# Performance work log

Measured on AMD Instinct MI355X. Metric: run time of the kernel, lower is better.

## Reference

```python
import jax, jax.numpy as jnp
import numpy as np

N = 100000      # nodes
E = 1600000     # edges (before self-loops)
IN_C = 128
HID = 256
L = 4
EPS = 1e-5


def setup_inputs() -> dict:
    key = jax.random.key(0)
    ks = jax.random.split(key, 12)
    s = 0.05
    x = jax.random.normal(ks[0], (N, IN_C), dtype=jnp.float32)
    edge_index = jax.random.randint(ks[1], (2, E), 0, N, dtype=jnp.int64)
    enc_w = jax.random.normal(ks[2], (IN_C, HID), dtype=jnp.float32) * s
    enc_b = jnp.zeros((HID,), jnp.float32)
    conv_w = jax.random.normal(ks[3], (L, HID, HID), dtype=jnp.float32) * s
    conv_b = jnp.zeros((L, HID), jnp.float32)
    ln_g = jnp.ones((L, HID), jnp.float32)
    ln_b = jnp.zeros((L, HID), jnp.float32)
    lin1_w = jax.random.normal(ks[4], (HID, HID // 2), dtype=jnp.float32) * s
    lin1_b = jnp.zeros((HID // 2,), jnp.float32)
    lin2_w = jax.random.normal(ks[5], (HID // 2, 1), dtype=jnp.float32) * s
    lin2_b = jnp.zeros((1,), jnp.float32)
    return dict(x=x, edge_index=edge_index, enc_w=enc_w, enc_b=enc_b,
                conv_w=conv_w, conv_b=conv_b, ln_g=ln_g, ln_b=ln_b,
                lin1_w=lin1_w, lin1_b=lin1_b, lin2_w=lin2_w, lin2_b=lin2_b)


def _layer_norm(h, g, b):
    mu = jnp.mean(h, axis=-1, keepdims=True)
    var = jnp.mean(jnp.square(h - mu), axis=-1, keepdims=True)
    return (h - mu) * jax.lax.rsqrt(var + EPS) * g + b


def reference(x, edge_index, enc_w, enc_b, conv_w, conv_b, ln_g, ln_b,
              lin1_w, lin1_b, lin2_w, lin2_b):
    loops = jnp.arange(N, dtype=edge_index.dtype)
    row = jnp.concatenate([edge_index[0], loops])   # source
    col = jnp.concatenate([edge_index[1], loops])   # target
    # GCN symmetric norm with self-loop weight 1 (improved=False)
    deg = jax.ops.segment_sum(jnp.ones(row.shape[0], jnp.float32), col,
                              num_segments=N)
    dis = jnp.where(deg > 0, jax.lax.rsqrt(deg), 0.0)  # deg^-1/2, [N]

    h = x @ enc_w + enc_b
    for i in range(L):
        hw = h @ conv_w[i]
        # norm_e = dis[row]*dis[col]: scale at source, aggregate, scale at target
        agg = jax.ops.segment_sum((hw * dis[:, None])[row], col,
                                  num_segments=N)
        h = agg * dis[:, None] + conv_b[i]
        h = jax.nn.relu(_layer_norm(h, ln_g[i], ln_b[i]))
        # dropout p=0.1 is identity in eval mode
    h = jax.nn.relu(h @ lin1_w + lin1_b)
    return h @ lin2_w + lin2_b  # [N, 1]
```

## Files before the change

### kernel.cpp

```cpp
#include <hip/hip_runtime.h>

#define N_NODES 100000
#define N_EDGES 1600000
#define IN_C    128
#define HID     256
#define NLAYER  4

#define NBUCK 391
#define BCAP  8192
#define EPB   4096
#define CAPL  6144

typedef __attribute__((ext_vector_type(8))) __bf16 bf16x8;
typedef __attribute__((ext_vector_type(4))) float  floatx4;
typedef __attribute__((ext_vector_type(2))) float  floatx2;

__device__ inline unsigned short f2b(float f) {
    unsigned u = __builtin_bit_cast(unsigned, f);
    return (unsigned short)((u + 0x7fffu + ((u >> 16) & 1u)) >> 16);
}
__device__ inline floatx2 pkadd(floatx2 x, floatx2 y) {
    floatx2 r;
    asm("v_pk_add_f32 %0, %1, %2" : "=v"(r) : "v"(x), "v"(y));
    return r;
}
__device__ inline void acc8p(floatx2* a, uint4 v) {
    unsigned wds[4] = {v.x, v.y, v.z, v.w};
    #pragma unroll
    for (int k = 0; k < 4; ++k) {
        floatx2 x;
        x[0] = __builtin_bit_cast(float, wds[k] << 16);
        x[1] = __builtin_bit_cast(float, wds[k] & 0xffff0000u);
        a[k] = pkadd(a[k], x);
    }
}
__device__ inline void gl16(const void* g, void* l) {
    __builtin_amdgcn_global_load_lds(
        (const __attribute__((address_space(1))) unsigned int*)g,
        (__attribute__((address_space(3))) unsigned int*)l, 16, 0, 0);
}

__global__ __launch_bounds__(256) void kb_scatter(
        const int* __restrict__ row, const int* __restrict__ col,
        int* __restrict__ gfill, unsigned* __restrict__ pairs, int e) {
    __shared__ unsigned sp[EPB];
    __shared__ unsigned short sbk[EPB];
    __shared__ int hist[NBUCK];
    __shared__ int lpre[NBUCK];
    __shared__ int lbase[NBUCK];
    __shared__ int wsum[4];
    __shared__ int carry;
    const int tid = threadIdx.x, lane = tid & 63, w = tid >> 6;
    const int base = blockIdx.x * EPB;
    const int nv   = min(EPB, e - base);
    for (int b = tid; b < NBUCK; b += 256) hist[b] = 0;
    __syncthreads();
    #pragma unroll
    for (int k = 0; k < EPB / 256; ++k) {
        int i = base + k * 256 + tid;
        if (i < e) atomicAdd(&hist[((unsigned)col[i]) >> 8], 1);
    }
    __syncthreads();
    for (int b = tid; b < NBUCK; b += 256) {
        int h = hist[b];
        lbase[b] = h ? atomicAdd(&gfill[b], h) : 0;
    }
    {
        int v = hist[tid];
        int inc = v;
        #pragma unroll
        for (int o = 1; o < 64; o <<= 1) { int u = __shfl_up(inc, o); if (lane >= o) inc += u; }
        if (lane == 63) wsum[w] = inc;
        __syncthreads();
        if (tid == 0) { int r = 0; for (int i = 0; i < 4; ++i) { int x = wsum[i]; wsum[i] = r; r += x; } carry = r; }
        __syncthreads();
        lpre[tid] = wsum[w] + inc - v;
        int c0 = carry;
        __syncthreads();
        int idx = 256 + tid;
        int v1 = (idx < NBUCK) ? hist[idx] : 0;
        int inc1 = v1;
        #pragma unroll
        for (int o = 1; o < 64; o <<= 1) { int u = __shfl_up(inc1, o); if (lane >= o) inc1 += u; }
        if (lane == 63) wsum[w] = inc1;
        __syncthreads();
        if (tid == 0) { int r = 0; for (int i = 0; i < 4; ++i) { int x = wsum[i]; wsum[i] = r; r += x; } }
        __syncthreads();
        if (idx < NBUCK) lpre[idx] = c0 + wsum[w] + inc1 - v1;
    }
    __syncthreads();
    for (int b = tid; b < NBUCK; b += 256) hist[b] = 0;
    __syncthreads();
    #pragma unroll
    for (int k = 0; k < EPB / 256; ++k) {
        int i = base + k * 256 + tid;
        if (i < e) {
            unsigned cv = (unsigned)col[i];
            int bk = cv >> 8;
            int q = lpre[bk] + atomicAdd(&hist[bk], 1);
            sp[q]  = ((unsigned)row[i] << 8) | (cv & 255u);
            sbk[q] = (unsigned short)bk;
        }
    }
    __syncthreads();
    for (int i = tid; i < nv; i += 256) {
        int bk = sbk[i];
        int pos = lbase[bk] + (i - lpre[bk]);
        if (pos < BCAP) pairs[(size_t)bk * BCAP + pos] = sp[i];
    }
}

__global__ __launch_bounds__(256) void kb_build(
        const unsigned* __restrict__ pairs, const int* __restrict__ gfill,
        int* __restrict__ offs, float* __restrict__ dis,
        int* __restrict__ srcl, int n) {
    __shared__ int lcnt[256];
    __shared__ int lstart[256];
    __shared__ int wsum[4];
    __shared__ int sbase;
    __shared__ int sl[CAPL];
    const int b = blockIdx.x;
    const int tid = threadIdx.x, lane = tid & 63, w = tid >> 6;
    int cnt = gfill[b]; if (cnt > CAPL) cnt = CAPL;
    const unsigned* bp = pairs + (size_t)b * BCAP;
    int pa = 0;
    for (int i = tid; i < b; i += 256) pa += gfill[i];
    #pragma unroll
    for (int o = 1; o < 64; o <<= 1) pa += __shfl_xor(pa, o);
    lcnt[tid] = 0;
    if (lane == 0) wsum[w] = pa;
    __syncthreads();
    if (tid == 0) sbase = wsum[0] + wsum[1] + wsum[2] + wsum[3];
    for (int i = tid; i < cnt; i += 256)
        atomicAdd(&lcnt[bp[i] & 255u], 1);
    __syncthreads();
    const int base = sbase;
    int v = lcnt[tid];
    int inc = v;
    #pragma unroll
    for (int o = 1; o < 64; o <<= 1) { int u = __shfl_up(inc, o); if (lane >= o) inc += u; }
    if (lane == 63) wsum[w] = inc;
    __syncthreads();
    if (tid == 0) { int r = 0; for (int i = 0; i < 4; ++i) { int x = wsum[i]; wsum[i] = r; r += x; } }
    __syncthreads();
    int excl = wsum[w] + inc - v;
    lstart[tid] = excl;
    int node = (b << 8) + tid;
    if (node < n) {
        dis[node]  = rsqrtf((float)(v + 1));
        offs[node] = base + excl;
    }
    __syncthreads();
    lcnt[tid] = 0;
    __syncthreads();
    for (int i = tid; i < cnt; i += 256) {
        unsigned pr = bp[i];
        int c = pr & 255u;
        int q = lstart[c] + atomicAdd(&lcnt[c], 1);
        sl[q] = (int)(pr >> 8);
    }
    __syncthreads();
    for (int i = tid; i < cnt; i += 256)
        srcl[base + i] = sl[i];
}

__global__ void k_wtz(const float* __restrict__ enc_w, const float* __restrict__ conv_w,
                      const float* __restrict__ w1,
                      unsigned short* __restrict__ enc_t, unsigned short* __restrict__ conv_t,
                      unsigned short* __restrict__ lin1_t, int* __restrict__ gfill,
                      int* __restrict__ offs) {
    int idx = blockIdx.x * blockDim.x + threadIdx.x;
    if (idx == 0) offs[N_NODES] = N_EDGES;
    if (idx < NBUCK) gfill[idx] = 0;
    if (idx < IN_C * HID) {
        int k = idx / HID, n = idx % HID;
        enc_t[n * IN_C + k] = f2b(enc_w[idx]);
    } else if (idx < IN_C * HID + NLAYER * HID * HID) {
        int r = idx - IN_C * HID;
        int l = r / (HID * HID);
        int e = r % (HID * HID);
        int k = e / HID, n = e % HID;
        conv_t[(size_t)l * HID * HID + n * HID + k] = f2b(conv_w[r]);
    } else if (idx < IN_C * HID + NLAYER * HID * HID + HID * (HID / 2)) {
        int e = idx - (IN_C * HID + NLAYER * HID * HID);
        int k = e / (HID / 2), n = e % (HID / 2);
        lin1_t[n * HID + k] = f2b(w1[e]);
    }
}

__global__ __launch_bounds__(512) void k_mme(
        const float* __restrict__ Af,
        const unsigned short* __restrict__ Wt,
        const float* __restrict__ bias,
        unsigned short* __restrict__ Cout, int M) {
    const int K = IN_C;
    __shared__ unsigned short As[128 * 32];
    __shared__ unsigned short Bs[256 * 32];
    const int tid  = threadIdx.x;
    const int lane = tid & 63;
    const int w    = tid >> 6;
    const int bm   = blockIdx.x * 128;

    const int r0 = tid >> 2, q0 = tid & 3;
    const int a_off  = min(bm + r0, M - 1) * K + q0 * 8;
    const int b_off0 = r0 * K + q0 * 8;
    const int b_off1 = (r0 + 128) * K + q0 * 8;

    floatx4 acc[4][4];
    #pragma unroll
    for (int i = 0; i < 4; ++i)
        #pragma unroll
        for (int j = 0; j < 4; ++j)
            acc[i][j] = (floatx4){0.f, 0.f, 0.f, 0.f};

    const int wm = (w & 1) * 64;
    const int wn = (w >> 1) * 64;
    const int fm = lane & 15;
    const int fq = (lane >> 4) * 8;

    uint4 ra;
    auto loadA = [&](int koff, uint4& oa) {
        float4 f0 = *(const float4*)(Af + a_off + koff);
        float4 f1 = *(const float4*)(Af + a_off + koff + 4);
        oa.x = (unsigned)f2b(f0.x) | ((unsigned)f2b(f0.y) << 16);
        oa.y = (unsigned)f2b(f0.z) | ((unsigned)f2b(f0.w) << 16);
        oa.z = (unsigned)f2b(f1.x) | ((unsigned)f2b(f1.y) << 16);
        oa.w = (unsigned)f2b(f1.z) | ((unsigned)f2b(f1.w) << 16);
    };

    loadA(0, ra);

    const int KT = K >> 5;
    for (int kt = 0; kt < KT; ++kt) {
        int k0 = kt << 5;
        ((uint4*)As)[tid] = ra;
        gl16(Wt + b_off0 + k0, Bs + (size_t)tid * 8);
        gl16(Wt + b_off1 + k0, Bs + (size_t)(tid + 512) * 8);
        __syncthreads();
        if (kt + 1 < KT) loadA((kt + 1) << 5, ra);
        bf16x8 af[4], bfr[4];
        #pragma unroll
        for (int i = 0; i < 4; ++i)
            af[i] = *(const bf16x8*)(const void*)(As + (wm + i * 16 + fm) * 32 + fq);
        #pragma unroll
        for (int j = 0; j < 4; ++j)
            bfr[j] = *(const bf16x8*)(const void*)(Bs + (wn + j * 16 + fm) * 32 + fq);
        #pragma unroll
        for (int i = 0; i < 4; ++i)
            #pragma unroll
            for (int j = 0; j < 4; ++j)
                acc[i][j] = __builtin_amdgcn_mfma_f32_16x16x32_bf16(af[i], bfr[j], acc[i][j], 0, 0, 0);
        __syncthreads();
    }

    const int quad = lane >> 4;
    #pragma unroll
    for (int i = 0; i < 4; ++i) {
        #pragma unroll
        for (int r = 0; r < 4; ++r) {
            int row = bm + wm + i * 16 + quad * 4 + r;
            if (row >= M) continue;
            #pragma unroll
            for (int j = 0; j < 4; ++j) {
                int colg = wn + j * 16 + fm;
                float v = acc[i][j][r] + bias[colg];
                Cout[(size_t)row * HID + colg] = f2b(v);
            }
        }
    }
}

__global__ __launch_bounds__(512) void k_mmc(
        const unsigned short* __restrict__ A,
        const unsigned short* __restrict__ Wt,
        const float* __restrict__ scale,
        unsigned short* __restrict__ Cout, int M) {
    const int K = HID;
    __shared__ unsigned short As[128 * 32];
    __shared__ unsigned short Bs[256 * 32];
    const int tid  = threadIdx.x;
    const int lane = tid & 63;
    const int w    = tid >> 6;
    const int bm   = blockIdx.x * 128;

    const int r0 = tid >> 2, q0 = tid & 3;
    const int a_off  = min(bm + r0, M - 1) * K + q0 * 8;
    const int b_off0 = r0 * K + q0 * 8;
    const int b_off1 = (r0 + 128) * K + q0 * 8;

    floatx4 acc[4][4];
    #pragma unroll
    for (int i = 0; i < 4; ++i)
        #pragma unroll
        for (int j = 0; j < 4; ++j)
            acc[i][j] = (floatx4){0.f, 0.f, 0.f, 0.f};

    const int wm = (w & 1) * 64;
    const int wn = (w >> 1) * 64;
    const int fm = lane & 15;
    const int fq = (lane >> 4) * 8;

    for (int kt = 0; kt < 8; ++kt) {
        int k0 = kt << 5;
        gl16(A  + a_off  + k0, As + (size_t)tid * 8);
        gl16(Wt + b_off0 + k0, Bs + (size_t)tid * 8);
        gl16(Wt + b_off1 + k0, Bs + (size_t)(tid + 512) * 8);
        __syncthreads();
        bf16x8 af[4], bfr[4];
        #pragma unroll
        for (int i = 0; i < 4; ++i)
            af[i] = *(const bf16x8*)(const void*)(As + (wm + i * 16 + fm) * 32 + fq);
        #pragma unroll
        for (int j = 0; j < 4; ++j)
            bfr[j] = *(const bf16x8*)(const void*)(Bs + (wn + j * 16 + fm) * 32 + fq);
        #pragma unroll
        for (int i = 0; i < 4; ++i)
            #pragma unroll
            for (int j = 0; j < 4; ++j)
                acc[i][j] = __builtin_amdgcn_mfma_f32_16x16x32_bf16(af[i], bfr[j], acc[i][j], 0, 0, 0);
        __syncthreads();
    }

    const int quad = lane >> 4;
    #pragma unroll
    for (int i = 0; i < 4; ++i) {
        #pragma unroll
        for (int r = 0; r < 4; ++r) {
            int row = bm + wm + i * 16 + quad * 4 + r;
            if (row >= M) continue;
            float sc = scale[row];
            #pragma unroll
            for (int j = 0; j < 4; ++j) {
                int colg = wn + j * 16 + fm;
                Cout[(size_t)row * HID + colg] = f2b(acc[i][j][r] * sc);
            }
        }
    }
}

__global__ __launch_bounds__(256) void k_head(
        const unsigned short* __restrict__ A,
        const unsigned short* __restrict__ Wt,
        const float* __restrict__ b1, const float* __restrict__ w2,
        const float* __restrict__ b2, float* __restrict__ out, int M) {
    const int K = 256;
    __shared__ unsigned short As[128 * 32];
    __shared__ unsigned short Bs[128 * 32];
    const int tid  = threadIdx.x;
    const int lane = tid & 63;
    const int w    = tid >> 6;
    const int bm   = blockIdx.x * 128;

    const int i0 = tid, i1 = tid + 256;
    const int r0 = i0 >> 2, r1 = i1 >> 2;
    const int q0 = i0 & 3,  q1 = i1 & 3;
    const int a_off0 = min(bm + r0, M - 1) * K + q0 * 8;
    const int a_off1 = min(bm + r1, M - 1) * K + q1 * 8;
    const int b_off0 = r0 * K + q0 * 8;
    const int b_off1 = r1 * K + q1 * 8;

    floatx4 acc[4][4];
    #pragma unroll
    for (int i = 0; i < 4; ++i)
        #pragma unroll
        for (int j = 0; j < 4; ++j)
            acc[i][j] = (floatx4){0.f, 0.f, 0.f, 0.f};

    const int wm = (w & 1) * 64;
    const int wn = (w >> 1) * 64;
    const int fm = lane & 15;
    const int fq = (lane >> 4) * 8;

    for (int kt = 0; kt < 8; ++kt) {
        int k0 = kt << 5;
        gl16(A  + a_off0 + k0, As + (size_t)i0 * 8);
        gl16(A  + a_off1 + k0, As + (size_t)i1 * 8);
        gl16(Wt + b_off0 + k0, Bs + (size_t)i0 * 8);
        gl16(Wt + b_off1 + k0, Bs + (size_t)i1 * 8);
        __syncthreads();
        bf16x8 af[4], bfr[4];
        #pragma unroll
        for (int i = 0; i < 4; ++i)
            af[i] = *(const bf16x8*)(const void*)(As + (wm + i * 16 + fm) * 32 + fq);
        #pragma unroll
        for (int j = 0; j < 4; ++j)
            bfr[j] = *(const bf16x8*)(const void*)(Bs + (wn + j * 16 + fm) * 32 + fq);
        #pragma unroll
        for (int i = 0; i < 4; ++i)
            #pragma unroll
            for (int j = 0; j < 4; ++j)
                acc[i][j] = __builtin_amdgcn_mfma_f32_16x16x32_bf16(af[i], bfr[j], acc[i][j], 0, 0, 0);
        __syncthreads();
    }

    float* red = (float*)As;
    const int q = lane >> 4;
    float b1v[4], w2v[4];
    #pragma unroll
    for (int j = 0; j < 4; ++j) {
        int col = wn + j * 16 + fm;
        b1v[j] = b1[col]; w2v[j] = w2[col];
    }
    #pragma unroll
    for (int i = 0; i < 4; ++i) {
        #pragma unroll
        for (int r = 0; r < 4; ++r) {
            float s = 0.f;
            #pragma unroll
            for (int j = 0; j < 4; ++j)
                s += fmaxf(acc[i][j][r] + b1v[j], 0.f) * w2v[j];
            #pragma unroll
            for (int off = 1; off < 16; off <<= 1) s += __shfl_xor(s, off);
            if (fm == 0) {
                int m = wm + i * 16 + q * 4 + r;
                red[m * 2 + (wn >> 6)] = s;
            }
        }
    }
    __syncthreads();
    if (tid < 128) {
        int row = bm + tid;
        if (row < M) out[row] = red[tid * 2] + red[tid * 2 + 1] + b2[0];
    }
}

__global__ void k_agg(const unsigned short* __restrict__ hw, const int* __restrict__ srcl,
                      const int* __restrict__ offs, const float* __restrict__ dis,
                      const float* __restrict__ cb, const float* __restrict__ g,
                      const float* __restrict__ bt, unsigned short* __restrict__ hout, int n) {
    int gtid = blockIdx.x * blockDim.x + threadIdx.x;
    int node = __builtin_amdgcn_readfirstlane(gtid >> 6);
    int lane = threadIdx.x & 63;
    const int half = lane >> 5;
    const int sub  = lane & 31;
    const uint4* T = (const uint4*)hw;

    floatx2 a2[4], c2[4];
    #pragma unroll
    for (int k = 0; k < 4; ++k) { a2[k] = (floatx2)0.f; c2[k] = (floatx2)0.f; }
    if (half == 0)
        acc8p(a2, T[(size_t)node * 32 + sub]);

    int p = offs[node], pe = offs[node + 1];
    if (p + 7 < pe) {
        uint4 va, vb, vc, vd;
        {
            int s0 = srcl[p],     s1 = srcl[p + 1], s2 = srcl[p + 2], s3 = srcl[p + 3];
            int s4 = srcl[p + 4], s5 = srcl[p + 5], s6 = srcl[p + 6], s7 = srcl[p + 7];
            int ea = half ? s1 : s0, eb = half ? s3 : s2;
            int ec = half ? s5 : s4, ed = half ? s7 : s6;
            va = T[(size_t)ea * 32 + sub]; vb = T[(size_t)eb * 32 + sub];
            vc = T[(size_t)ec * 32 + sub]; vd = T[(size_t)ed * 32 + sub];
        }
        for (p += 8; p + 7 < pe; p += 8) {
            int s0 = srcl[p],     s1 = srcl[p + 1], s2 = srcl[p + 2], s3 = srcl[p + 3];
            int s4 = srcl[p + 4], s5 = srcl[p + 5], s6 = srcl[p + 6], s7 = srcl[p + 7];
            int ea = half ? s1 : s0, eb = half ? s3 : s2;
            int ec = half ? s5 : s4, ed = half ? s7 : s6;
            uint4 wa = T[(size_t)ea * 32 + sub];
            uint4 wb = T[(size_t)eb * 32 + sub];
            uint4 wc = T[(size_t)ec * 32 + sub];
            uint4 wd = T[(size_t)ed * 32 + sub];
            acc8p(a2, va); acc8p(c2, vb); acc8p(a2, vc); acc8p(c2, vd);
            va = wa; vb = wb; vc = wc; vd = wd;
        }
        acc8p(a2, va); acc8p(c2, vb); acc8p(a2, vc); acc8p(c2, vd);
    }
    for (; p + 1 < pe; p += 2) {
        int s0 = srcl[p], s1 = srcl[p + 1];
        int ea = half ? s1 : s0;
        acc8p(a2, T[(size_t)ea * 32 + sub]);
    }
    if (p < pe && half == 0)
        acc8p(a2, T[(size_t)srcl[p] * 32 + sub]);

    float af[8];
    #pragma unroll
    for (int k = 0; k < 4; ++k) {
        floatx2 t = pkadd(a2[k], c2[k]);
        af[2 * k]     = t[0] + __shfl_xor(t[0], 32);
        af[2 * k + 1] = t[1] + __shfl_xor(t[1], 32);
    }
    float dc = dis[node];
    const float4* cb4 = (const float4*)cb;
    const float4* g4  = (const float4*)g;
    const float4* bt4 = (const float4*)bt;
    float4 cba = cb4[sub * 2], cbb = cb4[sub * 2 + 1];
    float h[8];
    h[0] = fmaf(af[0], dc, cba.x); h[1] = fmaf(af[1], dc, cba.y);
    h[2] = fmaf(af[2], dc, cba.z); h[3] = fmaf(af[3], dc, cba.w);
    h[4] = fmaf(af[4], dc, cbb.x); h[5] = fmaf(af[5], dc, cbb.y);
    h[6] = fmaf(af[6], dc, cbb.z); h[7] = fmaf(af[7], dc, cbb.w);
    float s = 0.f, sq = 0.f;
    #pragma unroll
    for (int j = 0; j < 8; ++j) { s += h[j]; sq += h[j] * h[j]; }
    #pragma unroll
    for (int off = 1; off < 32; off <<= 1) { s += __shfl_xor(s, off); sq += __shfl_xor(sq, off); }
    float mu  = s * (1.f / 256.f);
    float var = sq * (1.f / 256.f) - mu * mu;
    float inv = rsqrtf(var + 1e-5f);
    if (half == 0) {
        float4 ga = g4[sub * 2], gb = g4[sub * 2 + 1];
        float4 ba = bt4[sub * 2], bb = bt4[sub * 2 + 1];
        float gv[8] = {ga.x, ga.y, ga.z, ga.w, gb.x, gb.y, gb.z, gb.w};
        float bv[8] = {ba.x, ba.y, ba.z, ba.w, bb.x, bb.y, bb.z, bb.w};
        unsigned short o[8];
        #pragma unroll
        for (int j = 0; j < 8; ++j)
            o[j] = f2b(fmaxf(fmaf((h[j] - mu) * inv, gv[j], bv[j]), 0.f));
        uint4 st;
        st.x = (unsigned)o[0] | ((unsigned)o[1] << 16);
        st.y = (unsigned)o[2] | ((unsigned)o[3] << 16);
        st.z = (unsigned)o[4] | ((unsigned)o[5] << 16);
        st.w = (unsigned)o[6] | ((unsigned)o[7] << 16);
        ((uint4*)hout)[(size_t)node * 32 + sub] = st;
    }
}

extern "C" void kernel_launch(void* const* d_in, const int* in_sizes, int n_in,
                              void* d_out, int out_size, void* d_ws, size_t ws_size,
                              hipStream_t stream) {
    const float* x      = (const float*)d_in[0];
    const int*   ei     = (const int*)d_in[1];
    const float* enc_w  = (const float*)d_in[2];
    const float* enc_b  = (const float*)d_in[3];
    const float* conv_w = (const float*)d_in[4];
    const float* conv_b = (const float*)d_in[5];
    const float* ln_g   = (const float*)d_in[6];
    const float* ln_b   = (const float*)d_in[7];
    const float* w1     = (const float*)d_in[8];
    const float* b1     = (const float*)d_in[9];
    const float* w2     = (const float*)d_in[10];
    const float* b2     = (const float*)d_in[11];
    float* out = (float*)d_out;

    char* ws = (char*)d_ws;
    size_t off = 0;
    auto alloc = [&](size_t bytes) -> void* {
        void* p = ws + off;
        off = (off + bytes + 255) & ~(size_t)255;
        return p;
    };
    int*   offs  = (int*)alloc((size_t)(N_NODES + 1) * 4);
    int*   srcl  = (int*)alloc((size_t)N_EDGES * 4);
    float* dis   = (float*)alloc((size_t)N_NODES * 4);
    int*   gfill = (int*)alloc((size_t)NBUCK * 4);
    unsigned short* hb = (unsigned short*)alloc((size_t)N_NODES * HID * 2);
    unsigned short* hw = (unsigned short*)alloc((size_t)N_NODES * HID * 2);
    unsigned* pairs = (unsigned*)alloc((size_t)NBUCK * BCAP * 4);
    unsigned short* enc_t  = (unsigned short*)alloc((size_t)IN_C * HID * 2);
    unsigned short* conv_t = (unsigned short*)alloc((size_t)NLAYER * HID * HID * 2);
    unsigned short* lin1_t = (unsigned short*)alloc((size_t)HID * (HID / 2) * 2);

    const int* row = ei;
    const int* col = ei + N_EDGES;

    {
        int tot = IN_C * HID + NLAYER * HID * HID + HID * (HID / 2);
        k_wtz<<<(tot + 255) / 256, 256, 0, stream>>>(enc_w, conv_w, w1,
                                                     enc_t, conv_t, lin1_t, gfill, offs);
    }
    kb_scatter<<<(N_EDGES + EPB - 1) / EPB, 256, 0, stream>>>(row, col, gfill, pairs, N_EDGES);
    kb_build<<<NBUCK, 256, 0, stream>>>(pairs, gfill, offs, dis, srcl, N_NODES);

    k_mme<<<(N_NODES + 127) / 128, 512, 0, stream>>>(x, enc_t, enc_b, hb, N_NODES);

    for (int l = 0; l < NLAYER; ++l) {
        k_mmc<<<(N_NODES + 127) / 128, 512, 0, stream>>>(
            hb, conv_t + (size_t)l * HID * HID, dis, hw, N_NODES);
        k_agg<<<(N_NODES * 64 + 255) / 256, 256, 0, stream>>>(
            hw, srcl, offs, dis, conv_b + l * HID, ln_g + l * HID, ln_b + l * HID, hb, N_NODES);
    }

    k_head<<<(N_NODES + 127) / 128, 256, 0, stream>>>(hb, lin1_t, b1, w2, b2, out, N_NODES);
}
```

Baseline: 787.2 us.

## Fuse aggregation+LayerNorm with next layer's GEMM via LDS-resident tile

Adds a k_fused kernel that gathers neighbor rows, applies bias, LayerNorm and ReLU for a 128-node tile, and stores the bf16 result in a swizzled 64 KB LDS tile. It then multiplies that tile by the next layer's weights with MFMA and writes the dis-scaled output. This removes the global write and re-read of the intermediate h between the aggregation and GEMM kernels for layers 1-3, using ping-pong buffers. The cost is lower occupancy from the large LDS footprint, and the gather phase runs one wave per node, serialized over 16 rows per block, which may hide gather latency less well than the standalone aggregation kernel.

```diff
diff --git a/kernel.cpp b/kernel.cpp
--- a/kernel.cpp
+++ b/kernel.cpp
@@ -338,6 +338,167 @@
     }
 }
 
+__global__ __launch_bounds__(512, 4) void k_fused(
+        const unsigned short* __restrict__ hwin, const int* __restrict__ srcl,
+        const int* __restrict__ offs, const float* __restrict__ dis,
+        const float* __restrict__ cb, const float* __restrict__ g,
+        const float* __restrict__ bt,
+        const unsigned short* __restrict__ Wt,
+        unsigned short* __restrict__ hwout, int M) {
+    __shared__ unsigned short As2[128 * 256];
+    __shared__ unsigned short Bs[256 * 32];
+    const int tid  = threadIdx.x;
+    const int lane = tid & 63;
+    const int w    = tid >> 6;
+    const int bm   = blockIdx.x * 128;
+    const int half = lane >> 5;
+    const int sub  = lane & 31;
+    const uint4* T = (const uint4*)hwin;
+    const float4* cb4 = (const float4*)cb;
+    const float4* g4  = (const float4*)g;
+    const float4* bt4 = (const float4*)bt;
+
+    for (int rr = 0; rr < 16; ++rr) {
+        const int nloc = rr * 8 + w;
+        const int node = bm + nloc;
+        if (node < M) {
+            floatx2 a2[4], c2[4];
+            #pragma unroll
+            for (int k = 0; k < 4; ++k) { a2[k] = (floatx2)0.f; c2[k] = (floatx2)0.f; }
+            if (half == 0)
+                acc8p(a2, T[(size_t)node * 32 + sub]);
+            int p = offs[node], pe = offs[node + 1];
+            if (p + 7 < pe) {
+                uint4 va, vb, vc, vd;
+                {
+                    int s0 = srcl[p],     s1 = srcl[p + 1], s2 = srcl[p + 2], s3 = srcl[p + 3];
+                    int s4 = srcl[p + 4], s5 = srcl[p + 5], s6 = srcl[p + 6], s7 = srcl[p + 7];
+                    int ea = half ? s1 : s0, eb = half ? s3 : s2;
+                    int ec = half ? s5 : s4, ed = half ? s7 : s6;
+                    va = T[(size_t)ea * 32 + sub]; vb = T[(size_t)eb * 32 + sub];
+                    vc = T[(size_t)ec * 32 + sub]; vd = T[(size_t)ed * 32 + sub];
+                }
+                for (p += 8; p + 7 < pe; p += 8) {
+                    int s0 = srcl[p],     s1 = srcl[p + 1], s2 = srcl[p + 2], s3 = srcl[p + 3];
+                    int s4 = srcl[p + 4], s5 = srcl[p + 5], s6 = srcl[p + 6], s7 = srcl[p + 7];
+                    int ea = half ? s1 : s0, eb = half ? s3 : s2;
+                    int ec = half ? s5 : s4, ed = half ? s7 : s6;
+                    uint4 wa = T[(size_t)ea * 32 + sub];
+                    uint4 wb = T[(size_t)eb * 32 + sub];
+                    uint4 wc = T[(size_t)ec * 32 + sub];
+                    uint4 wd = T[(size_t)ed * 32 + sub];
+                    acc8p(a2, va); acc8p(c2, vb); acc8p(a2, vc); acc8p(c2, vd);
+                    va = wa; vb = wb; vc = wc; vd = wd;
+                }
+                acc8p(a2, va); acc8p(c2, vb); acc8p(a2, vc); acc8p(c2, vd);
+            }
+            for (; p + 1 < pe; p += 2) {
+                int s0 = srcl[p], s1 = srcl[p + 1];
+                int ea = half ? s1 : s0;
+                acc8p(a2, T[(size_t)ea * 32 + sub]);
+            }
+            if (p < pe && half == 0)
+                acc8p(a2, T[(size_t)srcl[p] * 32 + sub]);
+
+            float af8[8];
+            #pragma unroll
+            for (int k = 0; k < 4; ++k) {
+                floatx2 t = pkadd(a2[k], c2[k]);
+                af8[2 * k]     = t[0] + __shfl_xor(t[0], 32);
+                af8[2 * k + 1] = t[1] + __shfl_xor(t[1], 32);
+            }
+            float dc = dis[node];
+            float4 cba = cb4[sub * 2], cbb = cb4[sub * 2 + 1];
+            float h[8];
+            h[0] = fmaf(af8[0], dc, cba.x); h[1] = fmaf(af8[1], dc, cba.y);
+            h[2] = fmaf(af8[2], dc, cba.z); h[3] = fmaf(af8[3], dc, cba.w);
+            h[4] = fmaf(af8[4], dc, cbb.x); h[5] = fmaf(af8[5], dc, cbb.y);
+            h[6] = fmaf(af8[6], dc, cbb.z); h[7] = fmaf(af8[7], dc, cbb.w);
+            float s = 0.f, sq = 0.f;
+            #pragma unroll
+            for (int j = 0; j < 8; ++j) { s += h[j]; sq += h[j] * h[j]; }
+            #pragma unroll
+            for (int off = 1; off < 32; off <<= 1) { s += __shfl_xor(s, off); sq += __shfl_xor(sq, off); }
+            float mu  = s * (1.f / 256.f);
+            float var = sq * (1.f / 256.f) - mu * mu;
+            float inv = rsqrtf(var + 1e-5f);
+            if (half == 0) {
+                float4 ga = g4[sub * 2], gb = g4[sub * 2 + 1];
+                float4 ba = bt4[sub * 2], bb = bt4[sub * 2 + 1];
+                float gv[8] = {ga.x, ga.y, ga.z, ga.w, gb.x, gb.y, gb.z, gb.w};
+                float bv[8] = {ba.x, ba.y, ba.z, ba.w, bb.x, bb.y, bb.z, bb.w};
+                unsigned short o[8];
+                #pragma unroll
+                for (int j = 0; j < 8; ++j)
+                    o[j] = f2b(fmaxf(fmaf((h[j] - mu) * inv, gv[j], bv[j]), 0.f));
+                uint4 st;
+                st.x = (unsigned)o[0] | ((unsigned)o[1] << 16);
+                st.y = (unsigned)o[2] | ((unsigned)o[3] << 16);
+                st.z = (unsigned)o[4] | ((unsigned)o[5] << 16);
+                st.w = (unsigned)o[6] | ((unsigned)o[7] << 16);
+                unsigned byte = ((unsigned)(nloc * 512 + sub * 16)) ^ (((unsigned)nloc & 7u) << 4);
+                *(uint4*)((char*)As2 + byte) = st;
+            }
+        }
+    }
+    __syncthreads();
+
+    const int r0 = tid >> 2, q0 = tid & 3;
+    const int b_off0 = r0 * 256 + q0 * 8;
+    const int b_off1 = (r0 + 128) * 256 + q0 * 8;
+
+    floatx4 acc[4][4];
+    #pragma unroll
+    for (int i = 0; i < 4; ++i)
+        #pragma unroll
+        for (int j = 0; j < 4; ++j)
+            acc[i][j] = (floatx4){0.f, 0.f, 0.f, 0.f};
+
+    const int wm = (w & 1) * 64;
+    const int wn = (w >> 1) * 64;
+    const int fm = lane & 15;
+    const int fq = (lane >> 4) * 8;
+
+    for (int kt = 0; kt < 8; ++kt) {
+        int k0 = kt << 5;
+        gl16(Wt + b_off0 + k0, Bs + (size_t)tid * 8);
+        gl16(Wt + b_off1 + k0, Bs + (size_t)(tid + 512) * 8);
+        __syncthreads();
+        bf16x8 af[4], bfr[4];
+        #pragma unroll
+        for (int i = 0; i < 4; ++i) {
+            int row = wm + i * 16 + fm;
+            unsigned byte = ((unsigned)(row * 512 + kt * 64 + fq * 2)) ^ (((unsigned)row & 7u) << 4);
+            af[i] = *(const bf16x8*)(const void*)((const char*)As2 + byte);
+        }
+        #pragma unroll
+        for (int j = 0; j < 4; ++j)
+            bfr[j] = *(const bf16x8*)(const void*)(Bs + (wn + j * 16 + fm) * 32 + fq);
+        #pragma unroll
+        for (int i = 0; i < 4; ++i)
+            #pragma unroll
+            for (int j = 0; j < 4; ++j)
+                acc[i][j] = __builtin_amdgcn_mfma_f32_16x16x32_bf16(af[i], bfr[j], acc[i][j], 0, 0, 0);
+        __syncthreads();
+    }
+
+    const int quad = lane >> 4;
+    #pragma unroll
+    for (int i = 0; i < 4; ++i) {
+        #pragma unroll
+        for (int r = 0; r < 4; ++r) {
+            int row = bm + wm + i * 16 + quad * 4 + r;
+            if (row >= M) continue;
+            float sc = dis[row];
+            #pragma unroll
+            for (int j = 0; j < 4; ++j) {
+                int colg = wn + j * 16 + fm;
+                hwout[(size_t)row * HID + colg] = f2b(acc[i][j][r] * sc);
+            }
+        }
+    }
+}
+
 __global__ __launch_bounds__(256) void k_head(
         const unsigned short* __restrict__ A,
         const unsigned short* __restrict__ Wt,
@@ -474,12 +635,12 @@
     if (p < pe && half == 0)
         acc8p(a2, T[(size_t)srcl[p] * 32 + sub]);
 
-    float af[8];
+    float af8[8];
     #pragma unroll
     for (int k = 0; k < 4; ++k) {
         floatx2 t = pkadd(a2[k], c2[k]);
-        af[2 * k]     = t[0] + __shfl_xor(t[0], 32);
-        af[2 * k + 1] = t[1] + __shfl_xor(t[1], 32);
+        af8[2 * k]     = t[0] + __shfl_xor(t[0], 32);
+        af8[2 * k + 1] = t[1] + __shfl_xor(t[1], 32);
     }
     float dc = dis[node];
     const float4* cb4 = (const float4*)cb;
@@ -487,10 +648,10 @@
     const float4* bt4 = (const float4*)bt;
     float4 cba = cb4[sub * 2], cbb = cb4[sub * 2 + 1];
     float h[8];
-    h[0] = fmaf(af[0], dc, cba.x); h[1] = fmaf(af[1], dc, cba.y);
-    h[2] = fmaf(af[2], dc, cba.z); h[3] = fmaf(af[3], dc, cba.w);
-    h[4] = fmaf(af[4], dc, cbb.x); h[5] = fmaf(af[5], dc, cbb.y);
-    h[6] = fmaf(af[6], dc, cbb.z); h[7] = fmaf(af[7], dc, cbb.w);
+    h[0] = fmaf(af8[0], dc, cba.x); h[1] = fmaf(af8[1], dc, cba.y);
+    h[2] = fmaf(af8[2], dc, cba.z); h[3] = fmaf(af8[3], dc, cba.w);
+    h[4] = fmaf(af8[4], dc, cbb.x); h[5] = fmaf(af8[5], dc, cbb.y);
+    h[6] = fmaf(af8[6], dc, cbb.z); h[7] = fmaf(af8[7], dc, cbb.w);
     float s = 0.f, sq = 0.f;
     #pragma unroll
     for (int j = 0; j < 8; ++j) { s += h[j]; sq += h[j] * h[j]; }
@@ -545,8 +706,9 @@
     int*   srcl  = (int*)alloc((size_t)N_EDGES * 4);
     float* dis   = (float*)alloc((size_t)N_NODES * 4);
     int*   gfill = (int*)alloc((size_t)NBUCK * 4);
-    unsigned short* hb = (unsigned short*)alloc((size_t)N_NODES * HID * 2);
-    unsigned short* hw = (unsigned short*)alloc((size_t)N_NODES * HID * 2);
+    unsigned short* hb  = (unsigned short*)alloc((size_t)N_NODES * HID * 2);
+    unsigned short* hwa = (unsigned short*)alloc((size_t)N_NODES * HID * 2);
+    unsigned short* hwb = (unsigned short*)alloc((size_t)N_NODES * HID * 2);
     unsigned* pairs = (unsigned*)alloc((size_t)NBUCK * BCAP * 4);
     unsigned short* enc_t  = (unsigned short*)alloc((size_t)IN_C * HID * 2);
     unsigned short* conv_t = (unsigned short*)alloc((size_t)NLAYER * HID * HID * 2);
@@ -563,14 +725,16 @@
     kb_scatter<<<(N_EDGES + EPB - 1) / EPB, 256, 0, stream>>>(row, col, gfill, pairs, N_EDGES);
     kb_build<<<NBUCK, 256, 0, stream>>>(pairs, gfill, offs, dis, srcl, N_NODES);
 
-    k_mme<<<(N_NODES + 127) / 128, 512, 0, stream>>>(x, enc_t, enc_b, hb, N_NODES);
-
-    for (int l = 0; l < NLAYER; ++l) {
-        k_mmc<<<(N_NODES + 127) / 128, 512, 0, stream>>>(
-            hb, conv_t + (size_t)l * HID * HID, dis, hw, N_NODES);
-        k_agg<<<(N_NODES * 64 + 255) / 256, 256, 0, stream>>>(
-            hw, srcl, offs, dis, conv_b + l * HID, ln_g + l * HID, ln_b + l * HID, hb, N_NODES);
-    }
-
-    k_head<<<(N_NODES + 127) / 128, 256, 0, stream>>>(hb, lin1_t, b1, w2, b2, out, N_NODES);
-}
+    const int gB = (N_NODES + 127) / 128;
+    k_mme<<<gB, 512, 0, stream>>>(x, enc_t, enc_b, hb, N_NODES);
+    k_mmc<<<gB, 512, 0, stream>>>(hb, conv_t, dis, hwa, N_NODES);
+    k_fused<<<gB, 512, 0, stream>>>(hwa, srcl, offs, dis, conv_b,           ln_g,           ln_b,
+                                    conv_t + (size_t)1 * HID * HID, hwb, N_NODES);
+    k_fused<<<gB, 512, 0, stream>>>(hwb, srcl, offs, dis, conv_b + HID,     ln_g + HID,     ln_b + HID,
+                                    conv_t + (size_t)2 * HID * HID, hwa, N_NODES);
+    k_fused<<<gB, 512, 0, stream>>>(hwa, srcl, offs, dis, conv_b + 2 * HID, ln_g + 2 * HID, ln_b + 2 * HID,
+                                    conv_t + (size_t)3 * HID * HID, hwb, N_NODES);
+    k_agg<<<(N_NODES * 64 + 255) / 256, 256, 0, stream>>>(
+        hwb, srcl, offs, dis, conv_b + 3 * HID, ln_g + 3 * HID, ln_b + 3 * HID, hb, N_NODES);
+    k_head<<<gB, 256, 0, stream>>>(hb, lin1_t, b1, w2, b2, out, N_NODES);
+}
```

After: 877.5 us. +11.5%, slower.
